# Kernel optimization log

Hardware: AMD Instinct MI355X
Metric: run time of the kernel (lower is better)

The kernel has to match this reference:

```python
import jax, jax.numpy as jnp
import numpy as np

EPS = 1e-12  # torch F.normalize default eps


def _l2_normalize(t):
    n = jnp.linalg.norm(t, axis=-1, keepdims=True)
    return t / jnp.maximum(n, EPS)


def _block(x, W, alpha):
    # x: [B,H,N,D]; W: [D,D] (torch Linear weight, applied as x @ W.T)
    xn = _l2_normalize(x)                                   # q_norm == k_norm (q=k=x)
    A = jnp.einsum('bhnd,bhmd->bhnm', xn, xn)               # cosine similarity [B,H,N,N]
    A = jax.nn.softmax(A / jnp.maximum(alpha, 0.01), axis=-1)
    av = jnp.einsum('bhnm,bhmd->bhnd', A, x)                # A @ v, v = x
    return jax.nn.relu(jnp.einsum('bhnd,ed->bhne', av, W) + x)


def setup_inputs() -> dict:
    key = jax.random.key(0)
    k1, k2, k3 = jax.random.split(key, 3)
    B, H, N, D = 4, 4, 4096, 64
    x = jax.random.normal(k1, (B, H, N, D), dtype=jnp.float32)
    # nn.Linear(dim, dim, bias=False) weights, kaiming-uniform-ish scale
    bound = 1.0 / np.sqrt(D)
    W1 = jax.random.uniform(k2, (D, D), dtype=jnp.float32, minval=-bound, maxval=bound)
    W2 = jax.random.uniform(k3, (D, D), dtype=jnp.float32, minval=-bound, maxval=bound)
    alpha1 = jnp.float32(1.0)
    alpha2 = jnp.float32(1.0)
    return {"x": x, "W1": W1, "W2": W2, "alpha1": alpha1, "alpha2": alpha2}


def reference(x, W1, W2, alpha1, alpha2):
    x = _block(x, W1, alpha1)
    x = _block(x, W2, alpha2)
    return x
```

## Files before the change

### kernel.cpp

```cpp
#include <hip/hip_runtime.h>

typedef unsigned short u16;
typedef unsigned int   u32;
typedef __bf16 bf16x8 __attribute__((ext_vector_type(8)));
typedef float  f32x16 __attribute__((ext_vector_type(16)));

#define BH    16
#define NSEQ  4096
#define DIM   64
#define BM    128
#define BN    64
#define LDP   72
#define NTH   32
#define QTILES (NSEQ / BM)

#define SK_OFF   0
#define SV_OFF   9216
#define SW_OFF   18432
#define LX_OFF   23040
#define SMEM_U16 23552
#define HBUF     4608

#define MFMA __builtin_amdgcn_mfma_f32_32x32x16_bf16

__device__ __forceinline__ float bf2f(u16 u) {
    union { u32 i; float f; } v; v.i = ((u32)u) << 16; return v.f;
}
__device__ __forceinline__ u16 f2bf(float f) {
    union { float f; u32 i; } v; v.f = f;
    u32 r = v.i + 0x7fffu + ((v.i >> 16) & 1u);
    return (u16)(r >> 16);
}
#if __has_builtin(__builtin_amdgcn_exp2f)
__device__ __forceinline__ float exp2_raw(float x) { return __builtin_amdgcn_exp2f(x); }
#else
__device__ __forceinline__ float exp2_raw(float x) {
    float r; asm("v_exp_f32 %0, %1" : "=v"(r) : "v"(x)); return r;
}
#endif
__device__ __forceinline__ u32 cvtpk(float a, float b) {
    u32 r; asm("v_cvt_pk_bf16_f32 %0, %1, %2" : "=v"(r) : "v"(a), "v"(b)); return r;
}
__device__ __forceinline__ void plswap(u32& a, u32& b) {
    asm("v_permlane32_swap_b32 %0, %1" : "+v"(a), "+v"(b));
}
__device__ __forceinline__ void lds_barrier() {
    asm volatile("s_waitcnt lgkmcnt(0)\n\ts_barrier" ::: "memory");
}
__device__ __forceinline__ bf16x8 ldq_scaled(const u16* p, float s) {
    union { u32 u[4]; bf16x8 v; } r;
#pragma unroll
    for (int i = 0; i < 4; i++)
        r.u[i] = cvtpk(bf2f(p[2*i]) * s, bf2f(p[2*i+1]) * s);
    return r.v;
}

__global__ __launch_bounds__(256) void ContentGCN_5059471475267_prepn(
    const float* __restrict__ src, u16* __restrict__ xn, u16* __restrict__ xr)
{
    int gid = blockIdx.x * 256 + threadIdx.x;
    int row = gid >> 2, cg = (gid & 3) * 16;
    size_t base = (size_t)row * DIM + cg;

    float v[16];
    const float4* g = (const float4*)(src + base);
#pragma unroll
    for (int i = 0; i < 4; i++) {
        float4 t = g[i];
        v[4*i] = t.x; v[4*i+1] = t.y; v[4*i+2] = t.z; v[4*i+3] = t.w;
    }
    float ss = 0.f;
#pragma unroll
    for (int d = 0; d < 16; d++) ss += v[d] * v[d];
    ss += __shfl_xor(ss, 1);
    ss += __shfl_xor(ss, 2);
    float n = sqrtf(ss);
    if (n < 1e-12f) n = 1e-12f;
    float inv = 1.0f / n;

    alignas(16) u16 nb[16], rb[16];
#pragma unroll
    for (int d = 0; d < 16; d++) { nb[d] = f2bf(v[d] * inv); rb[d] = f2bf(v[d]); }
    uint4* gn = (uint4*)(xn + base);
    gn[0] = ((uint4*)nb)[0]; gn[1] = ((uint4*)nb)[1];
    uint4* gr = (uint4*)(xr + base);
    gr[0] = ((uint4*)rb)[0]; gr[1] = ((uint4*)rb)[1];
}

__global__ __launch_bounds__(512, 4) void ContentGCN_5059471475267_attn(
    const u16* __restrict__ xn, const u16* __restrict__ vsrc,
    const void* __restrict__ res, int res_isf,
    const float* __restrict__ Wt, const float* __restrict__ alphap,
    void* __restrict__ outp, int out_isf, u16* __restrict__ xnout)
{
    __shared__ u16 smem[SMEM_U16];
    u16* sK = smem + SK_OFF;
    u16* sV = smem + SV_OFF;
    u16* sW = smem + SW_OFF;
    float* lX = (float*)(smem + LX_OFF);

    int tid  = threadIdx.x;
    int w    = tid >> 6, lane = tid & 63;
    int half = w >> 2,  wv   = w & 3;
    int l31  = lane & 31, hi = lane >> 5;
    int bh   = blockIdx.x >> 5;
    int qt   = blockIdx.x & 31;

    float scale = 1.4426950408889634f / fmaxf(alphap[0], 0.01f);

    {
        int rr = tid >> 3, c0 = (tid & 7) * 8;
        const float4* gw = (const float4*)(Wt + rr * DIM + c0);
        float4 t0 = gw[0], t1 = gw[1];
        alignas(16) u16 wb[8];
        wb[0] = f2bf(t0.x); wb[1] = f2bf(t0.y); wb[2] = f2bf(t0.z); wb[3] = f2bf(t0.w);
        wb[4] = f2bf(t1.x); wb[5] = f2bf(t1.y); wb[6] = f2bf(t1.z); wb[7] = f2bf(t1.w);
        *(uint4*)&sW[rr * LDP + c0] = *(const uint4*)wb;
    }

    int qrow = qt * BM + wv * 32 + l31;
    const u16* qp = xn + ((size_t)bh * NSEQ + qrow) * DIM + hi * 8;
    bf16x8 bQ0 = ldq_scaled(qp,      scale);
    bf16x8 bQ1 = ldq_scaled(qp + 16, scale);
    bf16x8 bQ2 = ldq_scaled(qp + 32, scale);
    bf16x8 bQ3 = ldq_scaled(qp + 48, scale);

    f32x16 z16;
#pragma unroll
    for (int i = 0; i < 16; i++) z16[i] = 0.f;
    f32x16 OT0 = z16, OT1 = z16;
    float la0 = 0.f, la1 = 0.f, la2 = 0.f, la3 = 0.f;

    u16* sKh = sK + half * HBUF;
    u16* sVh = sV + half * HBUF;

    int ltid = tid & 255;
    int srow = ltid >> 2, scol = (ltid & 3) * 16;
    int nl   = (srow + ((ltid & 3) << 4)) & 63;

    const u16* pk = xn   + ((size_t)bh * NSEQ + half * (NTH * BN) + srow) * DIM + scol;
    const u16* pv = vsrc + ((size_t)bh * NSEQ + half * (NTH * BN) + srow) * DIM + scol;
    uint4 ck0 = ((const uint4*)pk)[0], ck1 = ((const uint4*)pk)[1];
    uint4 cv0 = ((const uint4*)pv)[0], cv1 = ((const uint4*)pv)[1];
    pk += (size_t)BN * DIM; pv += (size_t)BN * DIM;

    const u16* kB = sKh + l31 * LDP + hi * 8;

    int g  = l31 >> 4;
    int r0 = ((g)     & 3) << 4;
    int r1 = ((g + 1) & 3) << 4;
    int r2 = ((g + 2) & 3) << 4;
    int r3 = ((g + 3) & 3) << 4;
    const u16* vA = sVh + l31 * LDP + hi * 8;
    const u16* vB = sVh + (32 + l31) * LDP + hi * 8;

    for (int kt = 0; kt < NTH; kt++) {
        lds_barrier();
        *(uint4*)&sKh[srow * LDP + scol]     = ck0;
        *(uint4*)&sKh[srow * LDP + scol + 8] = ck1;
        {
            alignas(16) u16 vb[16];
            ((uint4*)vb)[0] = cv0; ((uint4*)vb)[1] = cv1;
#pragma unroll
            for (int j = 0; j < 16; j++) sVh[(scol + j) * LDP + nl] = vb[j];
        }
        if (kt + 1 < NTH) {
            ck0 = ((const uint4*)pk)[0]; ck1 = ((const uint4*)pk)[1];
            cv0 = ((const uint4*)pv)[0]; cv1 = ((const uint4*)pv)[1];
            pk += (size_t)BN * DIM; pv += (size_t)BN * DIM;
        }
        lds_barrier();

        const u16* kb1 = kB + 32 * LDP;
        f32x16 ST0, ST1;
        __builtin_amdgcn_s_setprio(1);
        ST0 = MFMA(*(const bf16x8*)(kB),       bQ0, z16, 0, 0, 0);
        ST0 = MFMA(*(const bf16x8*)(kB + 16),  bQ1, ST0, 0, 0, 0);
        ST0 = MFMA(*(const bf16x8*)(kB + 32),  bQ2, ST0, 0, 0, 0);
        ST0 = MFMA(*(const bf16x8*)(kB + 48),  bQ3, ST0, 0, 0, 0);
        ST1 = MFMA(*(const bf16x8*)(kb1),      bQ0, z16, 0, 0, 0);
        ST1 = MFMA(*(const bf16x8*)(kb1 + 16), bQ1, ST1, 0, 0, 0);
        ST1 = MFMA(*(const bf16x8*)(kb1 + 32), bQ2, ST1, 0, 0, 0);
        ST1 = MFMA(*(const bf16x8*)(kb1 + 48), bQ3, ST1, 0, 0, 0);
        __builtin_amdgcn_s_setprio(0);

        {
            float p0  = exp2_raw(ST0[0]);
            float p1  = exp2_raw(ST0[1]);
            float p2  = exp2_raw(ST0[2]);
            float p3  = exp2_raw(ST0[3]);
            float p4  = exp2_raw(ST0[4]);
            float p5  = exp2_raw(ST0[5]);
            float p6  = exp2_raw(ST0[6]);
            float p7  = exp2_raw(ST0[7]);
            float p8  = exp2_raw(ST0[8]);
            float p9  = exp2_raw(ST0[9]);
            float p10 = exp2_raw(ST0[10]);
            float p11 = exp2_raw(ST0[11]);
            float p12 = exp2_raw(ST0[12]);
            float p13 = exp2_raw(ST0[13]);
            float p14 = exp2_raw(ST0[14]);
            float p15 = exp2_raw(ST0[15]);
            u32 w0 = cvtpk(p0,  p1),  w1 = cvtpk(p2,  p3);
            u32 w2 = cvtpk(p4,  p5),  w3 = cvtpk(p6,  p7);
            u32 w4 = cvtpk(p8,  p9),  w5 = cvtpk(p10, p11);
            u32 w6 = cvtpk(p12, p13), w7 = cvtpk(p14, p15);
            plswap(w0, w2); plswap(w1, w3);
            plswap(w4, w6); plswap(w5, w7);
            union { u32 u[4]; bf16x8 v; } bp0, bp1;
            bp0.u[0] = w0; bp0.u[1] = w1; bp0.u[2] = w2; bp0.u[3] = w3;
            bp1.u[0] = w4; bp1.u[1] = w5; bp1.u[2] = w6; bp1.u[3] = w7;
            __builtin_amdgcn_s_setprio(1);
            OT0 = MFMA(*(const bf16x8*)(vA + r0), bp0.v, OT0, 0, 0, 0);
            OT0 = MFMA(*(const bf16x8*)(vA + r1), bp1.v, OT0, 0, 0, 0);
            OT1 = MFMA(*(const bf16x8*)(vB + r2), bp0.v, OT1, 0, 0, 0);
            OT1 = MFMA(*(const bf16x8*)(vB + r3), bp1.v, OT1, 0, 0, 0);
            __builtin_amdgcn_s_setprio(0);
            la0 += (p0 + p4) + (p8  + p12);
            la1 += (p1 + p5) + (p9  + p13);
            la2 += (p2 + p6) + (p10 + p14);
            la3 += (p3 + p7) + (p11 + p15);
        }

        {
            float p0  = exp2_raw(ST1[0]);
            float p1  = exp2_raw(ST1[1]);
            float p2  = exp2_raw(ST1[2]);
            float p3  = exp2_raw(ST1[3]);
            float p4  = exp2_raw(ST1[4]);
            float p5  = exp2_raw(ST1[5]);
            float p6  = exp2_raw(ST1[6]);
            float p7  = exp2_raw(ST1[7]);
            float p8  = exp2_raw(ST1[8]);
            float p9  = exp2_raw(ST1[9]);
            float p10 = exp2_raw(ST1[10]);
            float p11 = exp2_raw(ST1[11]);
            float p12 = exp2_raw(ST1[12]);
            float p13 = exp2_raw(ST1[13]);
            float p14 = exp2_raw(ST1[14]);
            float p15 = exp2_raw(ST1[15]);
            u32 w0 = cvtpk(p0,  p1),  w1 = cvtpk(p2,  p3);
            u32 w2 = cvtpk(p4,  p5),  w3 = cvtpk(p6,  p7);
            u32 w4 = cvtpk(p8,  p9),  w5 = cvtpk(p10, p11);
            u32 w6 = cvtpk(p12, p13), w7 = cvtpk(p14, p15);
            plswap(w0, w2); plswap(w1, w3);
            plswap(w4, w6); plswap(w5, w7);
            union { u32 u[4]; bf16x8 v; } bp0, bp1;
            bp0.u[0] = w0; bp0.u[1] = w1; bp0.u[2] = w2; bp0.u[3] = w3;
            bp1.u[0] = w4; bp1.u[1] = w5; bp1.u[2] = w6; bp1.u[3] = w7;
            __builtin_amdgcn_s_setprio(1);
            OT0 = MFMA(*(const bf16x8*)(vA + r2), bp0.v, OT0, 0, 0, 0);
            OT0 = MFMA(*(const bf16x8*)(vA + r3), bp1.v, OT0, 0, 0, 0);
            OT1 = MFMA(*(const bf16x8*)(vB + r0), bp0.v, OT1, 0, 0, 0);
            OT1 = MFMA(*(const bf16x8*)(vB + r1), bp1.v, OT1, 0, 0, 0);
            __builtin_amdgcn_s_setprio(0);
            la0 += (p0 + p4) + (p8  + p12);
            la1 += (p1 + p5) + (p9  + p13);
            la2 += (p2 + p6) + (p10 + p14);
            la3 += (p3 + p7) + (p11 + p15);
        }
    }

    float lsum = (la0 + la1) + (la2 + la3);
    u32 ja = __float_as_uint(lsum), jb = ja;
    plswap(ja, jb);
    float lfull = __uint_as_float(ja) + __uint_as_float(jb);

    __syncthreads();
    if (lane < 32) lX[w * 32 + l31] = lfull;
    __syncthreads();
    float invl = 1.0f / (lfull + lX[(w ^ 4) * 32 + l31]);

    union { u32 u[4]; bf16x8 v; } av0, av1, av2, av3;
    {
        u32 x0 = cvtpk(OT0[0]  * invl, OT0[1]  * invl), x1 = cvtpk(OT0[2]  * invl, OT0[3]  * invl);
        u32 x2 = cvtpk(OT0[4]  * invl, OT0[5]  * invl), x3 = cvtpk(OT0[6]  * invl, OT0[7]  * invl);
        u32 x4 = cvtpk(OT0[8]  * invl, OT0[9]  * invl), x5 = cvtpk(OT0[10] * invl, OT0[11] * invl);
        u32 x6 = cvtpk(OT0[12] * invl, OT0[13] * invl), x7 = cvtpk(OT0[14] * invl, OT0[15] * invl);
        plswap(x0, x2); plswap(x1, x3); plswap(x4, x6); plswap(x5, x7);
        av0.u[0] = x0; av0.u[1] = x1; av0.u[2] = x2; av0.u[3] = x3;
        av1.u[0] = x4; av1.u[1] = x5; av1.u[2] = x6; av1.u[3] = x7;
        u32 y0 = cvtpk(OT1[0]  * invl, OT1[1]  * invl), y1 = cvtpk(OT1[2]  * invl, OT1[3]  * invl);
        u32 y2 = cvtpk(OT1[4]  * invl, OT1[5]  * invl), y3 = cvtpk(OT1[6]  * invl, OT1[7]  * invl);
        u32 y4 = cvtpk(OT1[8]  * invl, OT1[9]  * invl), y5 = cvtpk(OT1[10] * invl, OT1[11] * invl);
        u32 y6 = cvtpk(OT1[12] * invl, OT1[13] * invl), y7 = cvtpk(OT1[14] * invl, OT1[15] * invl);
        plswap(y0, y2); plswap(y1, y3); plswap(y4, y6); plswap(y5, y7);
        av2.u[0] = y0; av2.u[1] = y1; av2.u[2] = y2; av2.u[3] = y3;
        av3.u[0] = y4; av3.u[1] = y5; av3.u[2] = y6; av3.u[3] = y7;
    }

    f32x16 R0, R1;
    {
        const u16* w0p = sW + l31 * LDP + hi * 8;
        const u16* w1p = sW + (32 + l31) * LDP + hi * 8;
        R0 = MFMA(*(const bf16x8*)(w0p),      av0.v, z16, 0, 0, 0);
        R0 = MFMA(*(const bf16x8*)(w0p + 16), av1.v, R0,  0, 0, 0);
        R0 = MFMA(*(const bf16x8*)(w0p + 32), av2.v, R0,  0, 0, 0);
        R0 = MFMA(*(const bf16x8*)(w0p + 48), av3.v, R0,  0, 0, 0);
        R1 = MFMA(*(const bf16x8*)(w1p),      av0.v, z16, 0, 0, 0);
        R1 = MFMA(*(const bf16x8*)(w1p + 16), av1.v, R1,  0, 0, 0);
        R1 = MFMA(*(const bf16x8*)(w1p + 32), av2.v, R1,  0, 0, 0);
        R1 = MFMA(*(const bf16x8*)(w1p + 48), av3.v, R1,  0, 0, 0);
    }

    float* outS = (float*)smem;
    if (half == 0) {
#pragma unroll
        for (int r = 0; r < 16; r++) {
            int e0 = (r & 3) + 8 * (r >> 2) + 4 * hi;
            outS[e0 * 133 + wv * 32 + l31]        = R0[r];
            outS[(e0 + 32) * 133 + wv * 32 + l31] = R1[r];
        }
    }
    __syncthreads();
    if (half == 1) {
#pragma unroll
        for (int r = 0; r < 16; r++) {
            int e0 = (r & 3) + 8 * (r >> 2) + 4 * hi;
            outS[e0 * 133 + wv * 32 + l31]        += R0[r];
            outS[(e0 + 32) * 133 + wv * 32 + l31] += R1[r];
        }
    }
    __syncthreads();

    {
        int q = tid >> 2, c = tid & 3;
        size_t gbase = ((size_t)bh * NSEQ + qt * BM + q) * DIM + c * 16;
        float vv[16];
#pragma unroll
        for (int j = 0; j < 16; j++) vv[j] = outS[(c * 16 + j) * 133 + q];
        if (res_isf) {
            const float4* rp = (const float4*)((const float*)res + gbase);
#pragma unroll
            for (int i = 0; i < 4; i++) {
                float4 t = rp[i];
                vv[4*i] += t.x; vv[4*i+1] += t.y; vv[4*i+2] += t.z; vv[4*i+3] += t.w;
            }
        } else {
            alignas(16) u16 rb[16];
            const uint4* rp = (const uint4*)((const u16*)res + gbase);
            ((uint4*)rb)[0] = rp[0]; ((uint4*)rb)[1] = rp[1];
#pragma unroll
            for (int j = 0; j < 16; j++) vv[j] += bf2f(rb[j]);
        }
#pragma unroll
        for (int j = 0; j < 16; j++) vv[j] = (vv[j] < 0.f) ? 0.f : vv[j];
        if (out_isf) {
            float4* op = (float4*)((float*)outp + gbase);
#pragma unroll
            for (int i = 0; i < 4; i++)
                op[i] = make_float4(vv[4*i], vv[4*i+1], vv[4*i+2], vv[4*i+3]);
        } else {
            alignas(16) u16 ob[16];
#pragma unroll
            for (int j = 0; j < 16; j++) ob[j] = f2bf(vv[j]);
            uint4* op = (uint4*)((u16*)outp + gbase);
            op[0] = ((uint4*)ob)[0]; op[1] = ((uint4*)ob)[1];
        }
        if (xnout) {
            float ss = 0.f;
#pragma unroll
            for (int j = 0; j < 16; j++) ss += vv[j] * vv[j];
            ss += __shfl_xor(ss, 1);
            ss += __shfl_xor(ss, 2);
            float n = sqrtf(ss);
            if (n < 1e-12f) n = 1e-12f;
            float inv = 1.0f / n;
            alignas(16) u16 nb[16];
#pragma unroll
            for (int j = 0; j < 16; j++) nb[j] = f2bf(vv[j] * inv);
            uint4* gn = (uint4*)(xnout + gbase);
            gn[0] = ((uint4*)nb)[0]; gn[1] = ((uint4*)nb)[1];
        }
    }
}

extern "C" void kernel_launch(void* const* d_in, const int* in_sizes, int n_in,
                              void* d_out, int out_size, void* d_ws, size_t ws_size,
                              hipStream_t stream) {
    const float* x  = (const float*)d_in[0];
    const float* W1 = (const float*)d_in[1];
    const float* W2 = (const float*)d_in[2];
    const float* a1 = (const float*)d_in[3];
    const float* a2 = (const float*)d_in[4];
    float* outp = (float*)d_out;

    size_t elems = (size_t)BH * NSEQ * DIM;
    u16* xn1 = (u16*)d_ws;
    u16* xr  = xn1 + elems;
    u16* xn2 = xr + elems;
    u16* y1  = xn2 + elems;

    dim3 pgrid(1024), pblk(256);
    dim3 agrid(BH * QTILES), ablk(512);

    ContentGCN_5059471475267_prepn<<<pgrid, pblk, 0, stream>>>(x, xn1, xr);
    ContentGCN_5059471475267_attn<<<agrid, ablk, 0, stream>>>(
        xn1, xr, x, 1, W1, a1, y1, 0, xn2);
    ContentGCN_5059471475267_attn<<<agrid, ablk, 0, stream>>>(
        xn2, y1, y1, 0, W2, a2, outp, 1, nullptr);
}
```

Before: 239.0 us.

## Overlap next K/V tile LDS store with softmax by hoisting V fragment reads

All V fragments for the current tile are now read from LDS into registers right after the QK MFMAs. After a barrier, the next K/V tile is written into the same LDS buffer while the exp/convert/PV stage runs out of registers. This removes the LDS store from the front of each iteration and overlaps it with softmax and PV math. It costs eight extra bf16x8 register fragments per thread, which raises register pressure and may lower occupancy.

Result: slower. 387.7 us (+62.2%).

```diff
diff --git a/kernel.cpp b/kernel.cpp
--- a/kernel.cpp
+++ b/kernel.cpp
@@ -140,9 +140,6 @@
 
     const u16* pk = xn   + ((size_t)bh * NSEQ + half * (NTH * BN) + srow) * DIM + scol;
     const u16* pv = vsrc + ((size_t)bh * NSEQ + half * (NTH * BN) + srow) * DIM + scol;
-    uint4 ck0 = ((const uint4*)pk)[0], ck1 = ((const uint4*)pk)[1];
-    uint4 cv0 = ((const uint4*)pv)[0], cv1 = ((const uint4*)pv)[1];
-    pk += (size_t)BN * DIM; pv += (size_t)BN * DIM;
 
     const u16* kB = sKh + l31 * LDP + hi * 8;
 
@@ -154,21 +151,22 @@
     const u16* vA = sVh + l31 * LDP + hi * 8;
     const u16* vB = sVh + (32 + l31) * LDP + hi * 8;
 
+    uint4 ck0 = ((const uint4*)pk)[0], ck1 = ((const uint4*)pk)[1];
+    uint4 cv0 = ((const uint4*)pv)[0], cv1 = ((const uint4*)pv)[1];
+    pk += (size_t)BN * DIM; pv += (size_t)BN * DIM;
+    *(uint4*)&sKh[srow * LDP + scol]     = ck0;
+    *(uint4*)&sKh[srow * LDP + scol + 8] = ck1;
+    {
+        alignas(16) u16 vb[16];
+        ((uint4*)vb)[0] = cv0; ((uint4*)vb)[1] = cv1;
+#pragma unroll
+        for (int j = 0; j < 16; j++) sVh[(scol + j) * LDP + nl] = vb[j];
+    }
+    ck0 = ((const uint4*)pk)[0]; ck1 = ((const uint4*)pk)[1];
+    cv0 = ((const uint4*)pv)[0]; cv1 = ((const uint4*)pv)[1];
+    pk += (size_t)BN * DIM; pv += (size_t)BN * DIM;
+
     for (int kt = 0; kt < NTH; kt++) {
-        lds_barrier();
-        *(uint4*)&sKh[srow * LDP + scol]     = ck0;
-        *(uint4*)&sKh[srow * LDP + scol + 8] = ck1;
-        {
-            alignas(16) u16 vb[16];
-            ((uint4*)vb)[0] = cv0; ((uint4*)vb)[1] = cv1;
-#pragma unroll
-            for (int j = 0; j < 16; j++) sVh[(scol + j) * LDP + nl] = vb[j];
-        }
-        if (kt + 1 < NTH) {
-            ck0 = ((const uint4*)pk)[0]; ck1 = ((const uint4*)pk)[1];
-            cv0 = ((const uint4*)pv)[0]; cv1 = ((const uint4*)pv)[1];
-            pk += (size_t)BN * DIM; pv += (size_t)BN * DIM;
-        }
         lds_barrier();
 
         const u16* kb1 = kB + 32 * LDP;
@@ -183,6 +181,31 @@
         ST1 = MFMA(*(const bf16x8*)(kb1 + 32), bQ2, ST1, 0, 0, 0);
         ST1 = MFMA(*(const bf16x8*)(kb1 + 48), bQ3, ST1, 0, 0, 0);
         __builtin_amdgcn_s_setprio(0);
+
+        bf16x8 vf0 = *(const bf16x8*)(vA + r0);
+        bf16x8 vf1 = *(const bf16x8*)(vA + r1);
+        bf16x8 vf2 = *(const bf16x8*)(vA + r2);
+        bf16x8 vf3 = *(const bf16x8*)(vA + r3);
+        bf16x8 vf4 = *(const bf16x8*)(vB + r0);
+        bf16x8 vf5 = *(const bf16x8*)(vB + r1);
+        bf16x8 vf6 = *(const bf16x8*)(vB + r2);
+        bf16x8 vf7 = *(const bf16x8*)(vB + r3);
+
+        lds_barrier();
+
+        if (kt + 1 < NTH) {
+            *(uint4*)&sKh[srow * LDP + scol]     = ck0;
+            *(uint4*)&sKh[srow * LDP + scol + 8] = ck1;
+            alignas(16) u16 vb[16];
+            ((uint4*)vb)[0] = cv0; ((uint4*)vb)[1] = cv1;
+#pragma unroll
+            for (int j = 0; j < 16; j++) sVh[(scol + j) * LDP + nl] = vb[j];
+            if (kt + 2 < NTH) {
+                ck0 = ((const uint4*)pk)[0]; ck1 = ((const uint4*)pk)[1];
+                cv0 = ((const uint4*)pv)[0]; cv1 = ((const uint4*)pv)[1];
+                pk += (size_t)BN * DIM; pv += (size_t)BN * DIM;
+            }
+        }
 
         {
             float p0  = exp2_raw(ST0[0]);
@@ -211,10 +234,10 @@
             bp0.u[0] = w0; bp0.u[1] = w1; bp0.u[2] = w2; bp0.u[3] = w3;
             bp1.u[0] = w4; bp1.u[1] = w5; bp1.u[2] = w6; bp1.u[3] = w7;
             __builtin_amdgcn_s_setprio(1);
-            OT0 = MFMA(*(const bf16x8*)(vA + r0), bp0.v, OT0, 0, 0, 0);
-            OT0 = MFMA(*(const bf16x8*)(vA + r1), bp1.v, OT0, 0, 0, 0);
-            OT1 = MFMA(*(const bf16x8*)(vB + r2), bp0.v, OT1, 0, 0, 0);
-            OT1 = MFMA(*(const bf16x8*)(vB + r3), bp1.v, OT1, 0, 0, 0);
+            OT0 = MFMA(vf0, bp0.v, OT0, 0, 0, 0);
+            OT0 = MFMA(vf1, bp1.v, OT0, 0, 0, 0);
+            OT1 = MFMA(vf6, bp0.v, OT1, 0, 0, 0);
+            OT1 = MFMA(vf7, bp1.v, OT1, 0, 0, 0);
             __builtin_amdgcn_s_setprio(0);
             la0 += (p0 + p4) + (p8  + p12);
             la1 += (p1 + p5) + (p9  + p13);
@@ -249,10 +272,10 @@
             bp0.u[0] = w0; bp0.u[1] = w1; bp0.u[2] = w2; bp0.u[3] = w3;
             bp1.u[0] = w4; bp1.u[1] = w5; bp1.u[2] = w6; bp1.u[3] = w7;
             __builtin_amdgcn_s_setprio(1);
-            OT0 = MFMA(*(const bf16x8*)(vA + r2), bp0.v, OT0, 0, 0, 0);
-            OT0 = MFMA(*(const bf16x8*)(vA + r3), bp1.v, OT0, 0, 0, 0);
-            OT1 = MFMA(*(const bf16x8*)(vB + r0), bp0.v, OT1, 0, 0, 0);
-            OT1 = MFMA(*(const bf16x8*)(vB + r1), bp1.v, OT1, 0, 0, 0);
+            OT0 = MFMA(vf2, bp0.v, OT0, 0, 0, 0);
+            OT0 = MFMA(vf3, bp1.v, OT0, 0, 0, 0);
+            OT1 = MFMA(vf4, bp0.v, OT1, 0, 0, 0);
+            OT1 = MFMA(vf5, bp1.v, OT1, 0, 0, 0);
             __builtin_amdgcn_s_setprio(0);
             la0 += (p0 + p4) + (p8  + p12);
             la1 += (p1 + p5) + (p9  + p13);
```
